# Performance work log

Hardware: AMD Instinct MI355X
Metric: run time of the kernel (lower is better)

## Reference

```python
import jax, jax.numpy as jnp
import numpy as np

RADIUS = 4
SIGMA_1 = 5.0
SIGMA_2 = 1.0


def _gaussian_kernel(dtype):
    # norm.pdf(d)/norm.pdf(0) == exp(-d^2/2)
    x2 = jnp.linspace(-RADIUS, RADIUS, 2 * RADIUS + 1) ** 2
    dist = jnp.sqrt(x2[:, None] + x2[None, :]) / SIGMA_1
    return jnp.exp(-0.5 * dist ** 2).astype(dtype)  # [k, k]


def setup_inputs() -> dict:
    key = jax.random.key(0)
    k1, k2 = jax.random.split(key)
    labels = jax.random.uniform(k1, (16, 20, 256, 256), dtype=jnp.float32)
    inputs = jax.random.uniform(k2, (16, 3, 256, 256), dtype=jnp.float32)
    return {"labels": labels, "inputs": inputs}


def reference(labels, inputs):
    B, K, H, W = labels.shape
    kernel = _gaussian_kernel(labels.dtype)

    # per-class mean color: mean(inputs * probs, HW) / (mean(probs, HW) + 1e-5)
    pmean = jnp.mean(labels, axis=(2, 3))                           # [B, K]
    xmean = jnp.einsum('bchw,bkhw->bkc', inputs, labels) / (H * W)  # [B, K, C]
    class_mean = xmean / (pmean[..., None] + 1e-5)                  # [B, K, C]

    # diff = sum_c (x_c - m_c)^2, expanded to avoid a [B,K,C,H,W] intermediate
    x2sum = jnp.sum(inputs ** 2, axis=1)                            # [B, H, W]
    cross = jnp.einsum('bchw,bkc->bkhw', inputs, class_mean)        # [B, K, H, W]
    m2 = jnp.sum(class_mean ** 2, axis=-1)                          # [B, K]
    diff = x2sum[:, None] - 2.0 * cross + m2[:, :, None, None]      # [B, K, H, W]
    weights = jnp.exp(-(diff ** 2) / (SIGMA_2 ** 2))                # [B, K, H, W]

    def blur(x):  # single-channel gaussian conv, vectorized over B*K
        lhs = x.reshape(B * K, 1, H, W)
        rhs = kernel[None, None]  # [1, 1, k, k]
        y = jax.lax.conv_general_dilated(
            lhs, rhs, window_strides=(1, 1),
            padding=[(RADIUS, RADIUS), (RADIUS, RADIUS)],
            dimension_numbers=('NCHW', 'OIHW', 'NCHW'))
        return y.reshape(B, K, H, W)

    num = jnp.sum(labels * blur(labels * weights), axis=(0, 2, 3))  # [K]
    den = jnp.sum(labels * blur(weights), axis=(0, 2, 3))           # [K]
    loss = jnp.sum(jnp.abs(num / (den + 1e-6)))
    return jnp.asarray(K, labels.dtype) - loss
```

## Files before the change

kernel.cpp:

```cpp
#include <hip/hip_runtime.h>

#define B_ 16
#define K_ 20
#define C_ 3
#define H_ 256
#define W_ 256
#define HW_ (H_*W_)
#define RAD 4
#define TH_ 64

__global__ __launch_bounds__(256) void zero_ws_k(float* ws, int n) {
    int i = blockIdx.x * 256 + threadIdx.x;
    if (i < n) ws[i] = 0.f;
}

__global__ __launch_bounds__(256) void stats_k(const float* __restrict__ labels,
                                               const float* __restrict__ inputs,
                                               float* __restrict__ sums) {
    const int x = threadIdx.x;
    const int chunk = blockIdx.x;
    const int k = blockIdx.y;
    const int b = blockIdx.z;
    const int r0 = chunk * 64;
    const size_t lab_base = ((size_t)(b * K_ + k)) * HW_;
    const size_t in_base  = ((size_t)b) * C_ * HW_;
    float sl = 0.f, s0 = 0.f, s1 = 0.f, s2 = 0.f;
    for (int r = r0; r < r0 + 64; ++r) {
        int off = r * W_ + x;
        float l  = labels[lab_base + off];
        float i0 = inputs[in_base + off];
        float i1 = inputs[in_base + HW_ + off];
        float i2 = inputs[in_base + 2 * HW_ + off];
        sl += l; s0 += l * i0; s1 += l * i1; s2 += l * i2;
    }
    for (int o = 32; o > 0; o >>= 1) {
        sl += __shfl_down(sl, o); s0 += __shfl_down(s0, o);
        s1 += __shfl_down(s1, o); s2 += __shfl_down(s2, o);
    }
    __shared__ float rb[4][4];
    int wid = x >> 6, lane = x & 63;
    if (lane == 0) { rb[0][wid] = sl; rb[1][wid] = s0; rb[2][wid] = s1; rb[3][wid] = s2; }
    __syncthreads();
    if (x == 0) {
        int bk = b * K_ + k;
        atomicAdd(&sums[bk],               rb[0][0] + rb[0][1] + rb[0][2] + rb[0][3]);
        atomicAdd(&sums[B_*K_ + bk],       rb[1][0] + rb[1][1] + rb[1][2] + rb[1][3]);
        atomicAdd(&sums[2*B_*K_ + bk],     rb[2][0] + rb[2][1] + rb[2][2] + rb[2][3]);
        atomicAdd(&sums[3*B_*K_ + bk],     rb[3][0] + rb[3][1] + rb[3][2] + rb[3][3]);
    }
}

__global__ __launch_bounds__(256) void fused_k(const float* __restrict__ labels,
                                               const float* __restrict__ inputs,
                                               const float* __restrict__ sums,
                                               float* __restrict__ numden) {
    const int x = threadIdx.x;
    const int strip = blockIdx.x;
    const int k = blockIdx.y;
    const int b = blockIdx.z;
    const int bk = b * K_ + k;

    const float dn  = sums[bk] + 1e-5f * (float)HW_;
    const float cm0 = sums[B_*K_ + bk]   / dn;
    const float cm1 = sums[2*B_*K_ + bk] / dn;
    const float cm2 = sums[3*B_*K_ + bk] / dn;
    const float m2  = cm0*cm0 + cm1*cm1 + cm2*cm2;

    float g[9];
#pragma unroll
    for (int i = 0; i < 9; ++i) { float d = (float)(i - 4); g[i] = __expf(-d * d * (1.f / 50.f)); }

    __shared__ float svw[2][W_ + 2*RAD];
    __shared__ float svlw[2][W_ + 2*RAD];
    if (x < RAD) {
        svw[0][x] = 0.f;  svw[0][W_ + RAD + x] = 0.f;
        svw[1][x] = 0.f;  svw[1][W_ + RAD + x] = 0.f;
        svlw[0][x] = 0.f; svlw[0][W_ + RAD + x] = 0.f;
        svlw[1][x] = 0.f; svlw[1][W_ + RAD + x] = 0.f;
    }

    const size_t lab_base = ((size_t)bk) * HW_;
    const size_t in_base  = ((size_t)b) * C_ * HW_;
    const int r0 = strip * TH_;

    float wv[9], lwv[9], lab[9];

    auto load_row = [&](int gr, float& w_, float& lw_, float& l_) {
        w_ = 0.f; lw_ = 0.f; l_ = 0.f;
        if (gr >= 0 && gr < H_) {
            int off = gr * W_ + x;
            float l  = labels[lab_base + off];
            float i0 = inputs[in_base + off];
            float i1 = inputs[in_base + HW_ + off];
            float i2 = inputs[in_base + 2 * HW_ + off];
            float df = (i0*i0 + i1*i1 + i2*i2) - 2.f * (i0*cm0 + i1*cm1 + i2*cm2) + m2;
            float wgt = __expf(-df * df);
            w_ = wgt; lw_ = l * wgt; l_ = l;
        }
    };

#pragma unroll
    for (int i = 0; i < 8; ++i) load_row(r0 - RAD + i, wv[i], lwv[i], lab[i]);

    __syncthreads();

    float num = 0.f, den = 0.f;
    for (int rr = 0; rr < TH_; ++rr) {
        load_row(r0 + rr + RAD, wv[8], lwv[8], lab[8]);
        float a = 0.f, c = 0.f;
#pragma unroll
        for (int i = 0; i < 9; ++i) { a += g[i] * wv[i]; c += g[i] * lwv[i]; }
        const int bf = rr & 1;
        svw[bf][RAD + x]  = a;
        svlw[bf][RAD + x] = c;
        __syncthreads();
        float hw = 0.f, hlw = 0.f;
#pragma unroll
        for (int i = 0; i < 9; ++i) { hw += g[i] * svw[bf][x + i]; hlw += g[i] * svlw[bf][x + i]; }
        float lc = lab[4];
        num += lc * hlw; den += lc * hw;
#pragma unroll
        for (int i = 0; i < 8; ++i) { wv[i] = wv[i+1]; lwv[i] = lwv[i+1]; lab[i] = lab[i+1]; }
    }

    for (int o = 32; o > 0; o >>= 1) { num += __shfl_down(num, o); den += __shfl_down(den, o); }
    __shared__ float rb[2][4];
    int wid = x >> 6, lane = x & 63;
    __syncthreads();
    if (lane == 0) { rb[0][wid] = num; rb[1][wid] = den; }
    __syncthreads();
    if (x == 0) {
        atomicAdd(&numden[k],      rb[0][0] + rb[0][1] + rb[0][2] + rb[0][3]);
        atomicAdd(&numden[K_ + k], rb[1][0] + rb[1][1] + rb[1][2] + rb[1][3]);
    }
}

__global__ void finalize_k(const float* __restrict__ numden, float* __restrict__ out) {
    if (threadIdx.x == 0 && blockIdx.x == 0) {
        float loss = 0.f;
        for (int kk = 0; kk < K_; ++kk)
            loss += fabsf(numden[kk] / (numden[K_ + kk] + 1e-6f));
        out[0] = (float)K_ - loss;
    }
}

extern "C" void kernel_launch(void* const* d_in, const int* in_sizes, int n_in,
                              void* d_out, int out_size, void* d_ws, size_t ws_size,
                              hipStream_t stream) {
    const float* labels = (const float*)d_in[0];
    const float* inputs = (const float*)d_in[1];
    float* ws     = (float*)d_ws;
    float* sums   = ws;
    float* numden = ws + 4 * B_ * K_;
    const int nz = 4 * B_ * K_ + 2 * K_;

    zero_ws_k<<<(nz + 255) / 256, 256, 0, stream>>>(ws, nz);
    stats_k<<<dim3(4, K_, B_), 256, 0, stream>>>(labels, inputs, sums);
    fused_k<<<dim3(H_ / TH_, K_, B_), 256, 0, stream>>>(labels, inputs, sums, numden);
    finalize_k<<<1, 64, 0, stream>>>(numden, (float*)d_out);
}
```

Baseline: 204.5 us.

## Vectorize stats and fused blur, move horizontal pass to wave shuffles

Both kernels now use float4 loads with one wave covering a full 256-wide row, and the block index is remapped so the stats grid runs more, smaller row chunks. The fused kernel swaps the row order: it blurs horizontally with cross-lane shuffles inside each wave, then vertically across a 9-row register ring, which removes the shared-memory staging and the per-row __syncthreads. Each block now holds four classes, one per wave, so neighbouring waves read the same input rows, and strips shrink to 16 rows to give more parallelism. The cost is more recomputation of halo rows per strip, higher register pressure from the fully unrolled ring buffers, and a relaunched grid layout.

```diff
diff --git a/kernel.cpp b/kernel.cpp
--- a/kernel.cpp
+++ b/kernel.cpp
@@ -2,12 +2,20 @@
 
 #define B_ 16
 #define K_ 20
-#define C_ 3
 #define H_ 256
 #define W_ 256
 #define HW_ (H_*W_)
-#define RAD 4
-#define TH_ 64
+#define BK_ (B_*K_)
+#define S_ 16
+#define NSTRIP_ 16
+
+__device__ __forceinline__ float4 ld4(const float* p) { return *(const float4*)p; }
+__device__ __forceinline__ float4 zero4() { return make_float4(0.f, 0.f, 0.f, 0.f); }
+
+#define G0_ 0.72614903707f
+#define G1_ 0.83527021141f
+#define G2_ 0.92311634639f
+#define G3_ 0.98019867331f
 
 __global__ __launch_bounds__(256) void zero_ws_k(float* ws, int n) {
     int i = blockIdx.x * 256 + threadIdx.x;
@@ -17,121 +25,170 @@
 __global__ __launch_bounds__(256) void stats_k(const float* __restrict__ labels,
                                                const float* __restrict__ inputs,
                                                float* __restrict__ sums) {
-    const int x = threadIdx.x;
-    const int chunk = blockIdx.x;
-    const int k = blockIdx.y;
-    const int b = blockIdx.z;
-    const int r0 = chunk * 64;
-    const size_t lab_base = ((size_t)(b * K_ + k)) * HW_;
-    const size_t in_base  = ((size_t)b) * C_ * HW_;
+    int idx = blockIdx.x;
+    int low = idx & 7; int t1 = idx >> 3;
+    int k = t1 % K_; int bch = t1 / K_;
+    int bc = bch * 8 + low;
+    int chunk = bc & 15, b = bc >> 4;
+
+    int tid = threadIdx.x;
+    int rowi = tid >> 6;
+    int colo = (tid & 63) * 4;
+
+    const float* lrow = labels + ((size_t)(b * K_ + k)) * HW_;
+    const float* ip   = inputs + (size_t)b * 3 * HW_;
+
     float sl = 0.f, s0 = 0.f, s1 = 0.f, s2 = 0.f;
-    for (int r = r0; r < r0 + 64; ++r) {
-        int off = r * W_ + x;
-        float l  = labels[lab_base + off];
-        float i0 = inputs[in_base + off];
-        float i1 = inputs[in_base + HW_ + off];
-        float i2 = inputs[in_base + 2 * HW_ + off];
-        sl += l; s0 += l * i0; s1 += l * i1; s2 += l * i2;
-    }
+    int r0 = chunk * 16 + rowi;
+#pragma unroll
+    for (int it = 0; it < 4; ++it) {
+        int off = (r0 + it * 4) * W_ + colo;
+        float4 l  = ld4(lrow + off);
+        float4 a  = ld4(ip + off);
+        float4 bb = ld4(ip + HW_ + off);
+        float4 cc = ld4(ip + 2 * HW_ + off);
+        sl += (l.x + l.y) + (l.z + l.w);
+        s0 += l.x * a.x  + l.y * a.y  + l.z * a.z  + l.w * a.w;
+        s1 += l.x * bb.x + l.y * bb.y + l.z * bb.z + l.w * bb.w;
+        s2 += l.x * cc.x + l.y * cc.y + l.z * cc.z + l.w * cc.w;
+    }
+#pragma unroll
     for (int o = 32; o > 0; o >>= 1) {
-        sl += __shfl_down(sl, o); s0 += __shfl_down(s0, o);
-        s1 += __shfl_down(s1, o); s2 += __shfl_down(s2, o);
+        sl += __shfl_xor(sl, o); s0 += __shfl_xor(s0, o);
+        s1 += __shfl_xor(s1, o); s2 += __shfl_xor(s2, o);
     }
     __shared__ float rb[4][4];
-    int wid = x >> 6, lane = x & 63;
-    if (lane == 0) { rb[0][wid] = sl; rb[1][wid] = s0; rb[2][wid] = s1; rb[3][wid] = s2; }
+    int wv = tid >> 6, lane = tid & 63;
+    if (lane == 0) { rb[0][wv] = sl; rb[1][wv] = s0; rb[2][wv] = s1; rb[3][wv] = s2; }
     __syncthreads();
-    if (x == 0) {
+    if (tid == 0) {
         int bk = b * K_ + k;
-        atomicAdd(&sums[bk],               rb[0][0] + rb[0][1] + rb[0][2] + rb[0][3]);
-        atomicAdd(&sums[B_*K_ + bk],       rb[1][0] + rb[1][1] + rb[1][2] + rb[1][3]);
-        atomicAdd(&sums[2*B_*K_ + bk],     rb[2][0] + rb[2][1] + rb[2][2] + rb[2][3]);
-        atomicAdd(&sums[3*B_*K_ + bk],     rb[3][0] + rb[3][1] + rb[3][2] + rb[3][3]);
-    }
+        atomicAdd(&sums[bk],          rb[0][0] + rb[0][1] + rb[0][2] + rb[0][3]);
+        atomicAdd(&sums[BK_ + bk],    rb[1][0] + rb[1][1] + rb[1][2] + rb[1][3]);
+        atomicAdd(&sums[2*BK_ + bk],  rb[2][0] + rb[2][1] + rb[2][2] + rb[2][3]);
+        atomicAdd(&sums[3*BK_ + bk],  rb[3][0] + rb[3][1] + rb[3][2] + rb[3][3]);
+    }
+}
+
+__device__ __forceinline__ float4 hblur9(float4 vL, float4 v, float4 vR) {
+    const float G[9] = {G0_, G1_, G2_, G3_, 1.0f, G3_, G2_, G1_, G0_};
+    float w[12] = {vL.x, vL.y, vL.z, vL.w, v.x, v.y, v.z, v.w, vR.x, vR.y, vR.z, vR.w};
+    float4 o = zero4();
+#pragma unroll
+    for (int j = 0; j < 9; ++j) {
+        o.x += G[j] * w[j];     o.y += G[j] * w[j + 1];
+        o.z += G[j] * w[j + 2]; o.w += G[j] * w[j + 3];
+    }
+    return o;
 }
 
 __global__ __launch_bounds__(256) void fused_k(const float* __restrict__ labels,
                                                const float* __restrict__ inputs,
                                                const float* __restrict__ sums,
                                                float* __restrict__ numden) {
-    const int x = threadIdx.x;
-    const int strip = blockIdx.x;
-    const int k = blockIdx.y;
-    const int b = blockIdx.z;
-    const int bk = b * K_ + k;
-
-    const float dn  = sums[bk] + 1e-5f * (float)HW_;
-    const float cm0 = sums[B_*K_ + bk]   / dn;
-    const float cm1 = sums[2*B_*K_ + bk] / dn;
-    const float cm2 = sums[3*B_*K_ + bk] / dn;
-    const float m2  = cm0*cm0 + cm1*cm1 + cm2*cm2;
-
-    float g[9];
-#pragma unroll
-    for (int i = 0; i < 9; ++i) { float d = (float)(i - 4); g[i] = __expf(-d * d * (1.f / 50.f)); }
-
-    __shared__ float svw[2][W_ + 2*RAD];
-    __shared__ float svlw[2][W_ + 2*RAD];
-    if (x < RAD) {
-        svw[0][x] = 0.f;  svw[0][W_ + RAD + x] = 0.f;
-        svw[1][x] = 0.f;  svw[1][W_ + RAD + x] = 0.f;
-        svlw[0][x] = 0.f; svlw[0][W_ + RAD + x] = 0.f;
-        svlw[1][x] = 0.f; svlw[1][W_ + RAD + x] = 0.f;
-    }
-
-    const size_t lab_base = ((size_t)bk) * HW_;
-    const size_t in_base  = ((size_t)b) * C_ * HW_;
-    const int r0 = strip * TH_;
-
-    float wv[9], lwv[9], lab[9];
-
-    auto load_row = [&](int gr, float& w_, float& lw_, float& l_) {
-        w_ = 0.f; lw_ = 0.f; l_ = 0.f;
-        if (gr >= 0 && gr < H_) {
-            int off = gr * W_ + x;
-            float l  = labels[lab_base + off];
-            float i0 = inputs[in_base + off];
-            float i1 = inputs[in_base + HW_ + off];
-            float i2 = inputs[in_base + 2 * HW_ + off];
-            float df = (i0*i0 + i1*i1 + i2*i2) - 2.f * (i0*cm0 + i1*cm1 + i2*cm2) + m2;
-            float wgt = __expf(-df * df);
-            w_ = wgt; lw_ = l * wgt; l_ = l;
+    const float G[9] = {G0_, G1_, G2_, G3_, 1.0f, G3_, G2_, G1_, G0_};
+    int idx = blockIdx.x;
+    int low = idx & 7; int t1 = idx >> 3;
+    int kq = t1 % 5; int sbh = t1 / 5;
+    int sb = sbh * 8 + low;
+    int strip = sb & 15, b = sb >> 4;
+    int tid = threadIdx.x;
+    int lane = tid & 63, wv = tid >> 6;
+    int k = kq * 4 + wv;
+    int bk = b * K_ + k;
+
+    float dn  = sums[bk] + 1e-5f * (float)HW_;
+    float inv = 1.f / dn;
+    float cm0 = sums[BK_ + bk] * inv;
+    float cm1 = sums[2 * BK_ + bk] * inv;
+    float cm2 = sums[3 * BK_ + bk] * inv;
+    float m2  = cm0 * cm0 + cm1 * cm1 + cm2 * cm2;
+
+    const float* lrow = labels + (size_t)bk * HW_;
+    const float* i0p = inputs + (size_t)b * 3 * HW_;
+    const float* i1p = i0p + HW_;
+    const float* i2p = i0p + 2 * HW_;
+    const int colo = lane * 4;
+    const int r0 = strip * S_;
+
+    float4 hwr[9], hlr[9];
+
+    auto loadrow = [&](int t, float4& ohw, float4& ohl) {
+        if ((unsigned)t < (unsigned)H_) {
+            int off = t * W_ + colo;
+            float4 l  = ld4(lrow + off);
+            float4 a  = ld4(i0p + off);
+            float4 bb = ld4(i1p + off);
+            float4 cc = ld4(i2p + off);
+            float4 w4, lw4;
+            {
+                float x2 = a.x*a.x + bb.x*bb.x + cc.x*cc.x;
+                float cr = a.x*cm0 + bb.x*cm1 + cc.x*cm2;
+                float df = x2 - 2.f*cr + m2;
+                w4.x = __expf(-(df*df)); lw4.x = l.x * w4.x;
+            }
+            {
+                float x2 = a.y*a.y + bb.y*bb.y + cc.y*cc.y;
+                float cr = a.y*cm0 + bb.y*cm1 + cc.y*cm2;
+                float df = x2 - 2.f*cr + m2;
+                w4.y = __expf(-(df*df)); lw4.y = l.y * w4.y;
+            }
+            {
+                float x2 = a.z*a.z + bb.z*bb.z + cc.z*cc.z;
+                float cr = a.z*cm0 + bb.z*cm1 + cc.z*cm2;
+                float df = x2 - 2.f*cr + m2;
+                w4.z = __expf(-(df*df)); lw4.z = l.z * w4.z;
+            }
+            {
+                float x2 = a.w*a.w + bb.w*bb.w + cc.w*cc.w;
+                float cr = a.w*cm0 + bb.w*cm1 + cc.w*cm2;
+                float df = x2 - 2.f*cr + m2;
+                w4.w = __expf(-(df*df)); lw4.w = l.w * w4.w;
+            }
+            float4 wl, wr2, ll2, lr2;
+            wl.x  = __shfl_up(w4.x, 1);  wl.y  = __shfl_up(w4.y, 1);
+            wl.z  = __shfl_up(w4.z, 1);  wl.w  = __shfl_up(w4.w, 1);
+            wr2.x = __shfl_down(w4.x, 1); wr2.y = __shfl_down(w4.y, 1);
+            wr2.z = __shfl_down(w4.z, 1); wr2.w = __shfl_down(w4.w, 1);
+            ll2.x = __shfl_up(lw4.x, 1); ll2.y = __shfl_up(lw4.y, 1);
+            ll2.z = __shfl_up(lw4.z, 1); ll2.w = __shfl_up(lw4.w, 1);
+            lr2.x = __shfl_down(lw4.x, 1); lr2.y = __shfl_down(lw4.y, 1);
+            lr2.z = __shfl_down(lw4.z, 1); lr2.w = __shfl_down(lw4.w, 1);
+            if (lane == 0)  { wl  = zero4(); ll2 = zero4(); }
+            if (lane == 63) { wr2 = zero4(); lr2 = zero4(); }
+            ohw = hblur9(wl, w4, wr2);
+            ohl = hblur9(ll2, lw4, lr2);
+        } else {
+            ohw = zero4(); ohl = zero4();
         }
     };
 
 #pragma unroll
-    for (int i = 0; i < 8; ++i) load_row(r0 - RAD + i, wv[i], lwv[i], lab[i]);
-
-    __syncthreads();
-
-    float num = 0.f, den = 0.f;
-    for (int rr = 0; rr < TH_; ++rr) {
-        load_row(r0 + rr + RAD, wv[8], lwv[8], lab[8]);
-        float a = 0.f, c = 0.f;
-#pragma unroll
-        for (int i = 0; i < 9; ++i) { a += g[i] * wv[i]; c += g[i] * lwv[i]; }
-        const int bf = rr & 1;
-        svw[bf][RAD + x]  = a;
-        svlw[bf][RAD + x] = c;
-        __syncthreads();
-        float hw = 0.f, hlw = 0.f;
-#pragma unroll
-        for (int i = 0; i < 9; ++i) { hw += g[i] * svw[bf][x + i]; hlw += g[i] * svlw[bf][x + i]; }
-        float lc = lab[4];
-        num += lc * hlw; den += lc * hw;
-#pragma unroll
-        for (int i = 0; i < 8; ++i) { wv[i] = wv[i+1]; lwv[i] = lwv[i+1]; lab[i] = lab[i+1]; }
-    }
-
-    for (int o = 32; o > 0; o >>= 1) { num += __shfl_down(num, o); den += __shfl_down(den, o); }
-    __shared__ float rb[2][4];
-    int wid = x >> 6, lane = x & 63;
-    __syncthreads();
-    if (lane == 0) { rb[0][wid] = num; rb[1][wid] = den; }
-    __syncthreads();
-    if (x == 0) {
-        atomicAdd(&numden[k],      rb[0][0] + rb[0][1] + rb[0][2] + rb[0][3]);
-        atomicAdd(&numden[K_ + k], rb[1][0] + rb[1][1] + rb[1][2] + rb[1][3]);
+    for (int i = 0; i < 8; ++i) loadrow(r0 - 4 + i, hwr[i], hlr[i]);
+
+    float nx=0,ny=0,nz=0,nw=0, dx=0,dy=0,dz=0,dw=0;
+#pragma unroll
+    for (int rr = 0; rr < S_; ++rr) {
+        loadrow(r0 + rr + 4, hwr[(rr + 8) % 9], hlr[(rr + 8) % 9]);
+        float4 vw = zero4(), vl = zero4();
+#pragma unroll
+        for (int j = 0; j < 9; ++j) {
+            const float4& aw = hwr[(rr + j) % 9];
+            const float4& al = hlr[(rr + j) % 9];
+            vw.x += G[j]*aw.x; vw.y += G[j]*aw.y; vw.z += G[j]*aw.z; vw.w += G[j]*aw.w;
+            vl.x += G[j]*al.x; vl.y += G[j]*al.y; vl.z += G[j]*al.z; vl.w += G[j]*al.w;
+        }
+        float4 l = ld4(lrow + (r0 + rr) * W_ + colo);
+        nx += l.x*vl.x; ny += l.y*vl.y; nz += l.z*vl.z; nw += l.w*vl.w;
+        dx += l.x*vw.x; dy += l.y*vw.y; dz += l.z*vw.z; dw += l.w*vw.w;
+    }
+    float num = (nx + ny) + (nz + nw);
+    float den = (dx + dy) + (dz + dw);
+#pragma unroll
+    for (int o = 32; o > 0; o >>= 1) { num += __shfl_xor(num, o); den += __shfl_xor(den, o); }
+    if (lane == 0) {
+        atomicAdd(&numden[k], num);
+        atomicAdd(&numden[K_ + k], den);
     }
 }
 
@@ -151,11 +208,11 @@
     const float* inputs = (const float*)d_in[1];
     float* ws     = (float*)d_ws;
     float* sums   = ws;
-    float* numden = ws + 4 * B_ * K_;
-    const int nz = 4 * B_ * K_ + 2 * K_;
+    float* numden = ws + 4 * BK_;
+    const int nz = 4 * BK_ + 2 * K_;
 
     zero_ws_k<<<(nz + 255) / 256, 256, 0, stream>>>(ws, nz);
-    stats_k<<<dim3(4, K_, B_), 256, 0, stream>>>(labels, inputs, sums);
-    fused_k<<<dim3(H_ / TH_, K_, B_), 256, 0, stream>>>(labels, inputs, sums, numden);
+    stats_k<<<256 * K_, 256, 0, stream>>>(labels, inputs, sums);
+    fused_k<<<(NSTRIP_ * B_ * 5), 256, 0, stream>>>(labels, inputs, sums, numden);
     finalize_k<<<1, 64, 0, stream>>>(numden, (float*)d_out);
 }
```

Measured after the change: 290.8 us. 42.2% more time.
